# Performance work log

Measured on AMD Instinct MI355X. Metric: run time of the kernel, lower is better.

Reference implementation:

```python
import jax, jax.numpy as jnp
import numpy as np

L, B, S, H = 2, 32, 2048, 512  # layers, batch, src_len, hidden_size
D = 2 * H                      # feature dim of hidden / encoder_outputs


def setup_inputs() -> dict:
    key = jax.random.key(0)
    k1, k2, k3, k4, k5 = jax.random.split(key, 5)
    scale = 1.0 / np.sqrt(4 * H)
    return {
        "hidden": jax.random.normal(k1, (L, B, D), dtype=jnp.float32),
        "encoder_outputs": jax.random.normal(k2, (B, S, D), dtype=jnp.float32),
        "attn_w": jax.random.normal(k3, (H, 4 * H), dtype=jnp.float32) * scale,
        "attn_b": jax.random.normal(k4, (H,), dtype=jnp.float32) * scale,
        "v_w": jax.random.normal(k5, (1, H), dtype=jnp.float32) * (1.0 / np.sqrt(H)),
    }


def reference(hidden, encoder_outputs, attn_w, attn_b, v_w):
    # hidden: [L, B, D]; permute(1,0,2) then [:, -1, :] == last layer state [B, D]
    h = hidden[-1]  # [B, D]
    # Avoid materializing the [B,S,2D] concat: split attn_w into the block acting
    # on the (repeated) hidden part and the block acting on encoder_outputs.
    w_h, w_e = attn_w[:, :D], attn_w[:, D:]          # [H, D] each
    # hidden contribution is constant over src_len -> compute once per batch row
    e_h = jnp.einsum('bd,hd->bh', h, w_h)            # [B, H]
    e_e = jnp.einsum('bsd,hd->bsh', encoder_outputs, w_e)  # [B, S, H]
    energy = jnp.tanh(e_e + e_h[:, None, :] + attn_b)      # [B, S, H]
    scores = jnp.einsum('bsh,h->bs', energy, v_w[0])       # [B, S]
    attention_weights = jax.nn.softmax(scores, axis=1)     # [B, S]
    context = jnp.einsum('bs,bsd->bd', attention_weights, encoder_outputs)
    return (context[:, None, :], attention_weights[:, None, :])
```

## Files before the change

### kernel.cpp

```cpp
#include <hip/hip_runtime.h>
#include <math.h>

#define LL 2
#define BB 32
#define SS 2048
#define HH 512
#define DD 1024
#define W4S 2048

#define BM 128
#define BN 512
#define BK 64
#define NT (DD / BK)
#define ASTR 72

typedef __attribute__((ext_vector_type(8))) short bf16x8;
typedef __attribute__((ext_vector_type(4))) float f32x4;

__device__ inline unsigned pk2_rne(float a, float b) {
    unsigned ua = __float_as_uint(a), ub = __float_as_uint(b);
    unsigned ra = (ua + 0x7fffu + ((ua >> 16) & 1u)) >> 16;
    unsigned rb = (ub + 0x7fffu + ((ub >> 16) & 1u)) & 0xffff0000u;
    return ra | rb;
}

__device__ inline unsigned pk2_hu(float a, float b) {
    unsigned ua = __float_as_uint(a) + 0x8000u;
    unsigned ub = __float_as_uint(b) + 0x8000u;
    return __builtin_amdgcn_perm(ub, ua, 0x07060302u);
}

__device__ inline float fast_tanh(float x) {
    x = fminf(9.f, fmaxf(-9.f, x));
    float e = __expf(2.f * x);
    return 1.f - 2.f * __builtin_amdgcn_rcpf(e + 1.f);
}

__device__ inline void gl_lds16(const unsigned short* g, short* l) {
    __builtin_amdgcn_global_load_lds(
        (const __attribute__((address_space(1))) unsigned int*)g,
        (__attribute__((address_space(3))) unsigned int*)l, 16, 0, 0);
}

__global__ __launch_bounds__(256) void k_pack(const float* __restrict__ attn_w,
                                              unsigned short* __restrict__ Bp,
                                              float* __restrict__ den) {
    int h = blockIdx.x, t = threadIdx.x;
    if (h == 0 && t < BB) den[t] = 0.f;
    float4 v = *(const float4*)(attn_w + (size_t)h * W4S + DD + t * 4);
    uint2 r = make_uint2(pk2_rne(v.x, v.y), pk2_rne(v.z, v.w));
    *(uint2*)(Bp + (size_t)h * DD + t * 4) = r;
}

__global__ __launch_bounds__(256) void k_base(const float* __restrict__ hidden,
                                              const float* __restrict__ attn_w,
                                              const float* __restrict__ attn_b,
                                              float* __restrict__ base) {
    int wid  = (blockIdx.x * 256 + threadIdx.x) >> 6;
    int lane = threadIdx.x & 63;
    int b = wid >> 9;
    int h = wid & (HH - 1);
    const float4* h4 = (const float4*)(hidden + (size_t)(LL - 1) * BB * DD + (size_t)b * DD);
    const float4* w4 = (const float4*)(attn_w + (size_t)h * W4S);
    float s = 0.f;
    #pragma unroll
    for (int i = 0; i < 4; i++) {
        float4 a = h4[lane + i * 64], w = w4[lane + i * 64];
        s += a.x * w.x + a.y * w.y + a.z * w.z + a.w * w.w;
    }
    #pragma unroll
    for (int off = 32; off; off >>= 1) s += __shfl_xor(s, off);
    if (lane == 0) base[b * HH + h] = s + attn_b[h];
}

__global__ __launch_bounds__(512, 2) void k_scores(const float* __restrict__ enc,
                                                   const unsigned short* __restrict__ Bp,
                                                   const float* __restrict__ base,
                                                   const float* __restrict__ vw,
                                                   float* __restrict__ den,
                                                   float* __restrict__ part,
                                                   float* __restrict__ attn_out) {
    __shared__ short As[BM * ASTR];
    __shared__ short Bs[2][BN * BK];

    const int tid  = threadIdx.x;
    const int wid  = tid >> 6;
    const int lane = tid & 63;
    const int lm   = lane & 15;
    const int kq   = lane >> 4;
    const int wr   = wid >> 2;
    const int wc   = wid & 3;
    const int m0   = blockIdx.x * BM;
    const int b    = m0 >> 11;
    const int srow = m0 & (SS - 1);
    const int wn   = wid * 64;

    const int rowA = tid >> 3;
    const int gA   = tid & 7;
    const float* Ag0 = enc + (size_t)(m0 + rowA) * DD + gA * 8;
    const float* Ag1 = Ag0 + (size_t)64 * DD;
    short* AsW0 = As + rowA * ASTR + gA * 8;
    short* AsW1 = AsW0 + 64 * ASTR;

    const int brow = lane >> 3;
    const int bgsw = (lane & 7) ^ brow;
    const unsigned short* Bg = Bp + (size_t)(wn + brow) * DD + bgsw * 8;

    f32x4 acc[4][8];
    #pragma unroll
    for (int i = 0; i < 4; i++)
        #pragma unroll
        for (int j = 0; j < 8; j++) acc[i][j] = (f32x4){0.f, 0.f, 0.f, 0.f};

    #pragma unroll
    for (int i = 0; i < 8; i++)
        gl_lds16(Bg + (size_t)(i * 8) * DD, &Bs[0][(wn + i * 8) * BK]);
    float4 a0 = *(const float4*)(Ag0);
    float4 a1 = *(const float4*)(Ag0 + 4);
    float4 a2 = *(const float4*)(Ag1);
    float4 a3 = *(const float4*)(Ag1 + 4);

    for (int kt = 0; kt < NT; kt++) {
        __syncthreads();
        uint4 p0 = {pk2_hu(a0.x, a0.y), pk2_hu(a0.z, a0.w),
                    pk2_hu(a1.x, a1.y), pk2_hu(a1.z, a1.w)};
        uint4 p1 = {pk2_hu(a2.x, a2.y), pk2_hu(a2.z, a2.w),
                    pk2_hu(a3.x, a3.y), pk2_hu(a3.z, a3.w)};
        *(uint4*)AsW0 = p0;
        *(uint4*)AsW1 = p1;
        __syncthreads();
        if (kt + 1 < NT) {
            #pragma unroll
            for (int i = 0; i < 8; i++)
                gl_lds16(Bg + (size_t)(i * 8) * DD + (kt + 1) * BK,
                         &Bs[(kt + 1) & 1][(wn + i * 8) * BK]);
            a0 = *(const float4*)(Ag0 + (kt + 1) * BK);
            a1 = *(const float4*)(Ag0 + (kt + 1) * BK + 4);
            a2 = *(const float4*)(Ag1 + (kt + 1) * BK);
            a3 = *(const float4*)(Ag1 + (kt + 1) * BK + 4);
        }
        const short* Bb = Bs[kt & 1];
        #pragma unroll
        for (int s = 0; s < 2; s++) {
            bf16x8 af[4];
            #pragma unroll
            for (int mi = 0; mi < 4; mi++)
                af[mi] = *(const bf16x8*)&As[(wr * 64 + mi * 16 + lm) * ASTR + (s * 4 + kq) * 8];
            #pragma unroll
            for (int ni = 0; ni < 8; ni++) {
                bf16x8 bf = *(const bf16x8*)
                    &Bb[(wc * 128 + ni * 16 + lm) * BK + (((s * 4 + kq)) ^ (lm & 7)) * 8];
                #pragma unroll
                for (int mi = 0; mi < 4; mi++)
                    acc[mi][ni] = __builtin_amdgcn_mfma_f32_16x16x32_bf16(
                        af[mi], bf, acc[mi][ni], 0, 0, 0);
            }
        }
    }

    __syncthreads();
    float* red  = (float*)As;
    float* esh  = red + 4 * BM;
    float* dsum = esh + BM;

    const float* basep = base + b * HH + wc * 128;
    const float* vp    = vw + wc * 128;
    float p[4][4] = {};
    #pragma unroll
    for (int ni = 0; ni < 8; ni++) {
        int nl = ni * 16 + lm;
        float bs = basep[nl];
        float vv = vp[nl];
        #pragma unroll
        for (int mi = 0; mi < 4; mi++)
            #pragma unroll
            for (int r = 0; r < 4; r++)
                p[mi][r] += vv * fast_tanh(acc[mi][ni][r] + bs);
    }
    #pragma unroll
    for (int off = 8; off; off >>= 1)
        #pragma unroll
        for (int mi = 0; mi < 4; mi++)
            #pragma unroll
            for (int r = 0; r < 4; r++)
                p[mi][r] += __shfl_xor(p[mi][r], off);
    if (lm == 0) {
        #pragma unroll
        for (int mi = 0; mi < 4; mi++)
            #pragma unroll
            for (int r = 0; r < 4; r++)
                red[wc * BM + wr * 64 + mi * 16 + kq * 4 + r] = p[mi][r];
    }
    __syncthreads();
    if (tid < BM) {
        float s = red[tid] + red[BM + tid] + red[2 * BM + tid] + red[3 * BM + tid];
        s = fminf(s, 80.f);
        float e = __expf(s);
        attn_out[b * SS + srow + tid] = e;
        esh[tid] = e;
        float rs = e;
        #pragma unroll
        for (int off = 32; off; off >>= 1) rs += __shfl_xor(rs, off);
        if ((tid & 63) == 0) dsum[tid >> 6] = rs;
    }
    __syncthreads();
    if (tid == 0) atomicAdd(den + b, dsum[0] + dsum[1]);

    const int half = tid >> 8;
    const int c4   = tid & 255;
    const float4* e4 = (const float4*)(enc + (size_t)(m0 + half * 64) * DD) + c4;
    float4 a = {0.f, 0.f, 0.f, 0.f};
    #pragma unroll 8
    for (int j = 0; j < 64; j++) {
        float w = esh[half * 64 + j];
        float4 ev = e4[(size_t)j * (DD / 4)];
        a.x += w * ev.x; a.y += w * ev.y;
        a.z += w * ev.z; a.w += w * ev.w;
    }
    *(float4*)(part + (size_t)(blockIdx.x * 2 + half) * DD + c4 * 4) = a;
}

__global__ __launch_bounds__(256) void k_finish(const float* __restrict__ part,
                                                const float* __restrict__ den,
                                                float* __restrict__ ctx,
                                                float* __restrict__ attn) {
    int b = blockIdx.x, y = blockIdx.y, t = threadIdx.x;
    float inv = 1.f / den[b];
    if (y < 4) {
        int d = y * 256 + t;
        float s = 0.f;
        #pragma unroll
        for (int j = 0; j < 32; j++) s += part[(size_t)(b * 32 + j) * DD + d];
        ctx[b * DD + d] = s * inv;
    } else {
        int sid = (y - 4) * 256 + t;
        attn[b * SS + sid] *= inv;
    }
}

extern "C" void kernel_launch(void* const* d_in, const int* in_sizes, int n_in,
                              void* d_out, int out_size, void* d_ws, size_t ws_size,
                              hipStream_t stream) {
    const float* hidden = (const float*)d_in[0];
    const float* enc    = (const float*)d_in[1];
    const float* attn_w = (const float*)d_in[2];
    const float* attn_b = (const float*)d_in[3];
    const float* v_w    = (const float*)d_in[4];

    float* out      = (float*)d_out;
    float* ctx_out  = out;
    float* attn_out = out + BB * DD;

    float* base = (float*)d_ws;
    float* den  = base + BB * HH;
    unsigned short* Bp = (unsigned short*)(den + 64);
    float* part = (float*)(Bp + (size_t)HH * DD);

    hipLaunchKernelGGL(k_pack, dim3(HH), dim3(256), 0, stream, attn_w, Bp, den);
    hipLaunchKernelGGL(k_base, dim3(BB * HH / 4), dim3(256), 0, stream,
                       hidden, attn_w, attn_b, base);
    hipLaunchKernelGGL(k_scores, dim3(BB * SS / BM), dim3(512), 0, stream,
                       enc, Bp, base, v_w, den, part, attn_out);
    hipLaunchKernelGGL(k_finish, dim3(BB, 12), dim3(256), 0, stream,
                       part, den, ctx_out, attn_out);
}
```

Baseline: 462.6 us.

## Load A directly to registers and pipeline B through a 4-stage LDS ring

New measurement: 510.6 us. 1.1x slower.

```diff
diff --git a/kernel.cpp b/kernel.cpp
--- a/kernel.cpp
+++ b/kernel.cpp
@@ -10,9 +10,8 @@
 
 #define BM 128
 #define BN 512
-#define BK 64
+#define BK 32
 #define NT (DD / BK)
-#define ASTR 72
 
 typedef __attribute__((ext_vector_type(8))) short bf16x8;
 typedef __attribute__((ext_vector_type(4))) float f32x4;
@@ -41,6 +40,8 @@
         (const __attribute__((address_space(1))) unsigned int*)g,
         (__attribute__((address_space(3))) unsigned int*)l, 16, 0, 0);
 }
+
+#define SB() __builtin_amdgcn_sched_barrier(0)
 
 __global__ __launch_bounds__(256) void k_pack(const float* __restrict__ attn_w,
                                               unsigned short* __restrict__ Bp,
@@ -73,6 +74,33 @@
     if (lane == 0) base[b * HH + h] = s + attn_b[h];
 }
 
+#define LOAD_A(KT) { _Pragma("unroll") for (int mi = 0; mi < 4; mi++) { \
+    pa[mi][0] = *(const float4*)(Ar + (size_t)mi * 16 * DD + (KT) * BK); \
+    pa[mi][1] = *(const float4*)(Ar + (size_t)mi * 16 * DD + (KT) * BK + 4); } }
+
+#define PACK_A() { _Pragma("unroll") for (int mi = 0; mi < 4; mi++) { \
+    uint4 u; u.x = pk2_hu(pa[mi][0].x, pa[mi][0].y); u.y = pk2_hu(pa[mi][0].z, pa[mi][0].w); \
+             u.z = pk2_hu(pa[mi][1].x, pa[mi][1].y); u.w = pk2_hu(pa[mi][1].z, pa[mi][1].w); \
+    af[mi] = *(bf16x8*)&u; } }
+
+#define PHASE_CORE(NH, ...) { \
+    __VA_ARGS__ \
+    bf16x8 b0 = *(const bf16x8*)&Bb[rb + ((NH) * 4 + 0) * 16 * BK]; \
+    bf16x8 b1 = *(const bf16x8*)&Bb[rb + ((NH) * 4 + 1) * 16 * BK]; \
+    bf16x8 b2 = *(const bf16x8*)&Bb[rb + ((NH) * 4 + 2) * 16 * BK]; \
+    bf16x8 b3 = *(const bf16x8*)&Bb[rb + ((NH) * 4 + 3) * 16 * BK]; \
+    SB(); __builtin_amdgcn_s_barrier(); SB(); \
+    __builtin_amdgcn_s_setprio(1); \
+    _Pragma("unroll") for (int mi = 0; mi < 4; mi++) { \
+        acc[mi][(NH) * 4 + 0] = __builtin_amdgcn_mfma_f32_16x16x32_bf16(af[mi], b0, acc[mi][(NH) * 4 + 0], 0, 0, 0); \
+        acc[mi][(NH) * 4 + 1] = __builtin_amdgcn_mfma_f32_16x16x32_bf16(af[mi], b1, acc[mi][(NH) * 4 + 1], 0, 0, 0); \
+        acc[mi][(NH) * 4 + 2] = __builtin_amdgcn_mfma_f32_16x16x32_bf16(af[mi], b2, acc[mi][(NH) * 4 + 2], 0, 0, 0); \
+        acc[mi][(NH) * 4 + 3] = __builtin_amdgcn_mfma_f32_16x16x32_bf16(af[mi], b3, acc[mi][(NH) * 4 + 3], 0, 0, 0); \
+    } \
+    __builtin_amdgcn_s_setprio(0); SB(); }
+
+#define ENDB() { __builtin_amdgcn_s_barrier(); SB(); }
+
 __global__ __launch_bounds__(512, 2) void k_scores(const float* __restrict__ enc,
                                                    const unsigned short* __restrict__ Bp,
                                                    const float* __restrict__ base,
@@ -80,8 +108,7 @@
                                                    float* __restrict__ den,
                                                    float* __restrict__ part,
                                                    float* __restrict__ attn_out) {
-    __shared__ short As[BM * ASTR];
-    __shared__ short Bs[2][BN * BK];
+    __shared__ short Bs[4][BN * BK];
 
     const int tid  = threadIdx.x;
     const int wid  = tid >> 6;
@@ -95,71 +122,60 @@
     const int srow = m0 & (SS - 1);
     const int wn   = wid * 64;
 
-    const int rowA = tid >> 3;
-    const int gA   = tid & 7;
-    const float* Ag0 = enc + (size_t)(m0 + rowA) * DD + gA * 8;
-    const float* Ag1 = Ag0 + (size_t)64 * DD;
-    short* AsW0 = As + rowA * ASTR + gA * 8;
-    short* AsW1 = AsW0 + 64 * ASTR;
-
-    const int brow = lane >> 3;
-    const int bgsw = (lane & 7) ^ brow;
+    const float* Ar = enc + (size_t)(m0 + wr * 64 + lm) * DD + kq * 8;
+
+    const int brow = lane >> 2;
+    const int bgsw = (lane & 3) ^ ((lane >> 3) & 3);
     const unsigned short* Bg = Bp + (size_t)(wn + brow) * DD + bgsw * 8;
 
+    const int rb = (wc * 128 + lm) * BK + (kq ^ ((lm >> 1) & 3)) * 8;
+
     f32x4 acc[4][8];
     #pragma unroll
     for (int i = 0; i < 4; i++)
         #pragma unroll
         for (int j = 0; j < 8; j++) acc[i][j] = (f32x4){0.f, 0.f, 0.f, 0.f};
 
-    #pragma unroll
-    for (int i = 0; i < 8; i++)
-        gl_lds16(Bg + (size_t)(i * 8) * DD, &Bs[0][(wn + i * 8) * BK]);
-    float4 a0 = *(const float4*)(Ag0);
-    float4 a1 = *(const float4*)(Ag0 + 4);
-    float4 a2 = *(const float4*)(Ag1);
-    float4 a3 = *(const float4*)(Ag1 + 4);
+    float4 pa[4][2];
+    bf16x8 af[4];
+
+    LOAD_A(0);
+    #pragma unroll
+    for (int i = 0; i < 4; i++)
+        gl_lds16(Bg + (size_t)(i * 16) * DD, &Bs[0][(wn + i * 16) * BK]);
+    #pragma unroll
+    for (int i = 0; i < 4; i++)
+        gl_lds16(Bg + (size_t)(i * 16) * DD + BK, &Bs[1][(wn + i * 16) * BK]);
+    asm volatile("s_waitcnt vmcnt(4)" ::: "memory");
+    SB();
+    __builtin_amdgcn_s_barrier();
+    SB();
 
     for (int kt = 0; kt < NT; kt++) {
-        __syncthreads();
-        uint4 p0 = {pk2_hu(a0.x, a0.y), pk2_hu(a0.z, a0.w),
-                    pk2_hu(a1.x, a1.y), pk2_hu(a1.z, a1.w)};
-        uint4 p1 = {pk2_hu(a2.x, a2.y), pk2_hu(a2.z, a2.w),
-                    pk2_hu(a3.x, a3.y), pk2_hu(a3.z, a3.w)};
-        *(uint4*)AsW0 = p0;
-        *(uint4*)AsW1 = p1;
-        __syncthreads();
-        if (kt + 1 < NT) {
-            #pragma unroll
-            for (int i = 0; i < 8; i++)
-                gl_lds16(Bg + (size_t)(i * 8) * DD + (kt + 1) * BK,
-                         &Bs[(kt + 1) & 1][(wn + i * 8) * BK]);
-            a0 = *(const float4*)(Ag0 + (kt + 1) * BK);
-            a1 = *(const float4*)(Ag0 + (kt + 1) * BK + 4);
-            a2 = *(const float4*)(Ag1 + (kt + 1) * BK);
-            a3 = *(const float4*)(Ag1 + (kt + 1) * BK + 4);
-        }
-        const short* Bb = Bs[kt & 1];
-        #pragma unroll
-        for (int s = 0; s < 2; s++) {
-            bf16x8 af[4];
-            #pragma unroll
-            for (int mi = 0; mi < 4; mi++)
-                af[mi] = *(const bf16x8*)&As[(wr * 64 + mi * 16 + lm) * ASTR + (s * 4 + kq) * 8];
-            #pragma unroll
-            for (int ni = 0; ni < 8; ni++) {
-                bf16x8 bf = *(const bf16x8*)
-                    &Bb[(wc * 128 + ni * 16 + lm) * BK + (((s * 4 + kq)) ^ (lm & 7)) * 8];
-                #pragma unroll
-                for (int mi = 0; mi < 4; mi++)
-                    acc[mi][ni] = __builtin_amdgcn_mfma_f32_16x16x32_bf16(
-                        af[mi], bf, acc[mi][ni], 0, 0, 0);
-            }
-        }
+        const short* Bb = Bs[kt & 3];
+        short* Bn = Bs[(kt + 2) & 3];
+        PACK_A();
+        PHASE_CORE(0,
+            if (kt + 1 < NT) { LOAD_A(kt + 1); }
+            if (kt + 2 < NT) {
+                gl_lds16(Bg + (size_t)0 * DD + (kt + 2) * BK, &Bn[(wn + 0) * BK]);
+                gl_lds16(Bg + (size_t)16 * DD + (kt + 2) * BK, &Bn[(wn + 16) * BK]);
+            } )
+        ENDB();
+        PHASE_CORE(1,
+            if (kt + 2 < NT) {
+                gl_lds16(Bg + (size_t)32 * DD + (kt + 2) * BK, &Bn[(wn + 32) * BK]);
+                gl_lds16(Bg + (size_t)48 * DD + (kt + 2) * BK, &Bn[(wn + 48) * BK]);
+            } )
+        if (kt + 2 < NT)      { asm volatile("s_waitcnt vmcnt(12)" ::: "memory"); }
+        else if (kt + 1 < NT) { asm volatile("s_waitcnt vmcnt(8)"  ::: "memory"); }
+        else                  { asm volatile("s_waitcnt vmcnt(0)"  ::: "memory"); }
+        SB();
+        ENDB();
     }
 
     __syncthreads();
-    float* red  = (float*)As;
+    float* red  = (float*)&Bs[0][0];
     float* esh  = red + 4 * BM;
     float* dsum = esh + BM;
 
```

## Feed encoder tile straight into registers for MFMA, dropping LDS A-staging

Applied to the files above, without the earlier changes.

Result: slower. 516.8 us (+11.7%).

```diff
diff --git a/kernel.cpp b/kernel.cpp
--- a/kernel.cpp
+++ b/kernel.cpp
@@ -8,11 +8,10 @@
 #define DD 1024
 #define W4S 2048
 
-#define BM 128
+#define BM 64
 #define BN 512
-#define BK 64
+#define BK 32
 #define NT (DD / BK)
-#define ASTR 72
 
 typedef __attribute__((ext_vector_type(8))) short bf16x8;
 typedef __attribute__((ext_vector_type(4))) float f32x4;
@@ -73,14 +72,22 @@
     if (lane == 0) base[b * HH + h] = s + attn_b[h];
 }
 
-__global__ __launch_bounds__(512, 2) void k_scores(const float* __restrict__ enc,
+#define LOAD_A(KT) { _Pragma("unroll") for (int mi = 0; mi < 4; mi++) { \
+    pa[mi][0] = *(const float4*)(Ar + (size_t)mi * 16 * DD + (KT) * BK); \
+    pa[mi][1] = *(const float4*)(Ar + (size_t)mi * 16 * DD + (KT) * BK + 4); } }
+
+#define PACK_A() { _Pragma("unroll") for (int mi = 0; mi < 4; mi++) { \
+    uint4 u; u.x = pk2_hu(pa[mi][0].x, pa[mi][0].y); u.y = pk2_hu(pa[mi][0].z, pa[mi][0].w); \
+             u.z = pk2_hu(pa[mi][1].x, pa[mi][1].y); u.w = pk2_hu(pa[mi][1].z, pa[mi][1].w); \
+    af[mi] = *(bf16x8*)&u; } }
+
+__global__ __launch_bounds__(256, 2) void k_scores(const float* __restrict__ enc,
                                                    const unsigned short* __restrict__ Bp,
                                                    const float* __restrict__ base,
                                                    const float* __restrict__ vw,
                                                    float* __restrict__ den,
                                                    float* __restrict__ part,
                                                    float* __restrict__ attn_out) {
-    __shared__ short As[BM * ASTR];
     __shared__ short Bs[2][BN * BK];
 
     const int tid  = threadIdx.x;
@@ -88,83 +95,69 @@
     const int lane = tid & 63;
     const int lm   = lane & 15;
     const int kq   = lane >> 4;
-    const int wr   = wid >> 2;
-    const int wc   = wid & 3;
     const int m0   = blockIdx.x * BM;
     const int b    = m0 >> 11;
     const int srow = m0 & (SS - 1);
-    const int wn   = wid * 64;
-
-    const int rowA = tid >> 3;
-    const int gA   = tid & 7;
-    const float* Ag0 = enc + (size_t)(m0 + rowA) * DD + gA * 8;
-    const float* Ag1 = Ag0 + (size_t)64 * DD;
-    short* AsW0 = As + rowA * ASTR + gA * 8;
-    short* AsW1 = AsW0 + 64 * ASTR;
-
-    const int brow = lane >> 3;
-    const int bgsw = (lane & 7) ^ brow;
+    const int wn   = wid << 7;
+
+    const float* Ar = enc + (size_t)(m0 + lm) * DD + kq * 8;
+
+    const int brow = lane >> 2;
+    const int bgsw = (lane & 3) ^ ((lane >> 3) & 3);
     const unsigned short* Bg = Bp + (size_t)(wn + brow) * DD + bgsw * 8;
 
+    const int rb = (wn + lm) * BK + (kq ^ ((lm >> 1) & 3)) * 8;
+
     f32x4 acc[4][8];
     #pragma unroll
     for (int i = 0; i < 4; i++)
         #pragma unroll
         for (int j = 0; j < 8; j++) acc[i][j] = (f32x4){0.f, 0.f, 0.f, 0.f};
 
+    float4 pa[4][2];
+    bf16x8 af[4];
+
     #pragma unroll
     for (int i = 0; i < 8; i++)
-        gl_lds16(Bg + (size_t)(i * 8) * DD, &Bs[0][(wn + i * 8) * BK]);
-    float4 a0 = *(const float4*)(Ag0);
-    float4 a1 = *(const float4*)(Ag0 + 4);
-    float4 a2 = *(const float4*)(Ag1);
-    float4 a3 = *(const float4*)(Ag1 + 4);
+        gl_lds16(Bg + (size_t)(i * 16) * DD, &Bs[0][(wn + i * 16) * BK]);
+    LOAD_A(0);
+    asm volatile("s_waitcnt vmcnt(8)" ::: "memory");
+    __builtin_amdgcn_s_barrier();
 
     for (int kt = 0; kt < NT; kt++) {
-        __syncthreads();
-        uint4 p0 = {pk2_hu(a0.x, a0.y), pk2_hu(a0.z, a0.w),
-                    pk2_hu(a1.x, a1.y), pk2_hu(a1.z, a1.w)};
-        uint4 p1 = {pk2_hu(a2.x, a2.y), pk2_hu(a2.z, a2.w),
-                    pk2_hu(a3.x, a3.y), pk2_hu(a3.z, a3.w)};
-        *(uint4*)AsW0 = p0;
-        *(uint4*)AsW1 = p1;
-        __syncthreads();
+        PACK_A();
         if (kt + 1 < NT) {
+            short* Bn = Bs[(kt + 1) & 1];
             #pragma unroll
             for (int i = 0; i < 8; i++)
-                gl_lds16(Bg + (size_t)(i * 8) * DD + (kt + 1) * BK,
-                         &Bs[(kt + 1) & 1][(wn + i * 8) * BK]);
-            a0 = *(const float4*)(Ag0 + (kt + 1) * BK);
-            a1 = *(const float4*)(Ag0 + (kt + 1) * BK + 4);
-            a2 = *(const float4*)(Ag1 + (kt + 1) * BK);
-            a3 = *(const float4*)(Ag1 + (kt + 1) * BK + 4);
+                gl_lds16(Bg + (size_t)(i * 16) * DD + (kt + 1) * BK,
+                         &Bn[(wn + i * 16) * BK]);
+            LOAD_A(kt + 1);
         }
+        __builtin_amdgcn_sched_barrier(0);
         const short* Bb = Bs[kt & 1];
-        #pragma unroll
-        for (int s = 0; s < 2; s++) {
-            bf16x8 af[4];
+        __builtin_amdgcn_s_setprio(1);
+        #pragma unroll
+        for (int ni = 0; ni < 8; ni++) {
+            bf16x8 bf = *(const bf16x8*)&Bb[rb + ni * 16 * BK];
             #pragma unroll
             for (int mi = 0; mi < 4; mi++)
-                af[mi] = *(const bf16x8*)&As[(wr * 64 + mi * 16 + lm) * ASTR + (s * 4 + kq) * 8];
-            #pragma unroll
-            for (int ni = 0; ni < 8; ni++) {
-                bf16x8 bf = *(const bf16x8*)
-                    &Bb[(wc * 128 + ni * 16 + lm) * BK + (((s * 4 + kq)) ^ (lm & 7)) * 8];
-                #pragma unroll
-                for (int mi = 0; mi < 4; mi++)
-                    acc[mi][ni] = __builtin_amdgcn_mfma_f32_16x16x32_bf16(
-                        af[mi], bf, acc[mi][ni], 0, 0, 0);
-            }
+                acc[mi][ni] = __builtin_amdgcn_mfma_f32_16x16x32_bf16(
+                    af[mi], bf, acc[mi][ni], 0, 0, 0);
         }
+        __builtin_amdgcn_s_setprio(0);
+        if (kt + 1 < NT) { asm volatile("s_waitcnt vmcnt(8)" ::: "memory"); }
+        else            { asm volatile("s_waitcnt vmcnt(0)" ::: "memory"); }
+        __builtin_amdgcn_s_barrier();
     }
 
     __syncthreads();
-    float* red  = (float*)As;
+    float* red  = (float*)&Bs[0][0];
     float* esh  = red + 4 * BM;
     float* dsum = esh + BM;
 
-    const float* basep = base + b * HH + wc * 128;
-    const float* vp    = vw + wc * 128;
+    const float* basep = base + b * HH + wn;
+    const float* vp    = vw + wn;
     float p[4][4] = {};
     #pragma unroll
     for (int ni = 0; ni < 8; ni++) {
@@ -189,7 +182,7 @@
         for (int mi = 0; mi < 4; mi++)
             #pragma unroll
             for (int r = 0; r < 4; r++)
-                red[wc * BM + wr * 64 + mi * 16 + kq * 4 + r] = p[mi][r];
+                red[wid * BM + mi * 16 + kq * 4 + r] = p[mi][r];
     }
     __syncthreads();
     if (tid < BM) {
@@ -201,23 +194,21 @@
         float rs = e;
         #pragma unroll
         for (int off = 32; off; off >>= 1) rs += __shfl_xor(rs, off);
-        if ((tid & 63) == 0) dsum[tid >> 6] = rs;
+        if (tid == 0) dsum[0] = rs;
     }
     __syncthreads();
-    if (tid == 0) atomicAdd(den + b, dsum[0] + dsum[1]);
-
-    const int half = tid >> 8;
-    const int c4   = tid & 255;
-    const float4* e4 = (const float4*)(enc + (size_t)(m0 + half * 64) * DD) + c4;
+    if (tid == 0) atomicAdd(den + b, dsum[0]);
+
+    const float4* e4 = (const float4*)(enc + (size_t)m0 * DD) + tid;
     float4 a = {0.f, 0.f, 0.f, 0.f};
     #pragma unroll 8
-    for (int j = 0; j < 64; j++) {
-        float w = esh[half * 64 + j];
+    for (int j = 0; j < BM; j++) {
+        float w = esh[j];
         float4 ev = e4[(size_t)j * (DD / 4)];
         a.x += w * ev.x; a.y += w * ev.y;
         a.z += w * ev.z; a.w += w * ev.w;
     }
-    *(float4*)(part + (size_t)(blockIdx.x * 2 + half) * DD + c4 * 4) = a;
+    *(float4*)(part + (size_t)blockIdx.x * DD + tid * 4) = a;
 }
 
 __global__ __launch_bounds__(256) void k_finish(const float* __restrict__ part,
@@ -259,7 +250,7 @@
     hipLaunchKernelGGL(k_pack, dim3(HH), dim3(256), 0, stream, attn_w, Bp, den);
     hipLaunchKernelGGL(k_base, dim3(BB * HH / 4), dim3(256), 0, stream,
                        hidden, attn_w, attn_b, base);
-    hipLaunchKernelGGL(k_scores, dim3(BB * SS / BM), dim3(512), 0, stream,
+    hipLaunchKernelGGL(k_scores, dim3(BB * SS / BM), dim3(256), 0, stream,
                        enc, Bp, base, v_w, den, part, attn_out);
     hipLaunchKernelGGL(k_finish, dim3(BB, 12), dim3(256), 0, stream,
                        part, den, ctx_out, attn_out);
```
